# Kernel optimization log

Measured on AMD Instinct MI355X. Metric: run time of the kernel, lower is better.

## Reference

```python
import jax, jax.numpy as jnp
import numpy as np


def setup_inputs() -> dict:
    key = jax.random.key(0)
    kq, kk, kv = jax.random.split(key, 3)
    B, H, T, D = 2, 8, 8192, 64
    return {
        "Q": jax.random.normal(kq, (B, H, T, D), dtype=jnp.float32),
        "K": jax.random.normal(kk, (B, H, T, D), dtype=jnp.float32),
        "V": jax.random.normal(kv, (B, H, T, D), dtype=jnp.float32),
        "window_size": 512,
    }


def _gather_bands(x, nb, Wn):
    # x: [B,H,T,D] -> [B,H,nb,3*Wn,D], key blocks (i-1, i, i+1) per query block i
    B, H, T, D = x.shape
    xb = x.reshape(B, H, nb, Wn, D)
    xp = jnp.pad(xb, ((0, 0), (0, 0), (1, 1), (0, 0), (0, 0)))
    return jnp.concatenate([xp[:, :, i:i + nb] for i in range(3)], axis=3)


def reference(Q, K, V, window_size):
    # Sliding-window attention: softmax over keys with |q_idx - kv_idx| <= window_size,
    # computed block-sparsely (only the 3 neighboring key blocks per query block).
    B, H, T, D = Q.shape
    Wn = int(window_size)
    assert T % Wn == 0
    nb = T // Wn
    scale = 1.0 / (D ** 0.5)

    Qb = Q.reshape(B, H, nb, Wn, D)
    Kw = _gather_bands(K, nb, Wn)  # [B,H,nb,3W,D]
    Vw = _gather_bands(V, nb, Wn)

    # scores within the band: [B,H,nb,W,3W]
    s = jnp.einsum('bhnqd,bhnkd->bhnqk', Qb, Kw) * scale

    # exact band mask: global q = n*W + q_loc, global kv = (n-1)*W + k_loc
    q_loc = jnp.arange(Wn)[:, None]
    k_loc = jnp.arange(3 * Wn)[None, :]
    band = jnp.abs(q_loc + Wn - k_loc) <= Wn          # [W, 3W]
    kv_g = (jnp.arange(nb)[:, None] - 1) * Wn + jnp.arange(3 * Wn)[None, :]  # [nb, 3W]
    valid = (kv_g >= 0) & (kv_g < T)
    mask = band[None, :, :] & valid[:, None, :]        # [nb, W, 3W]

    s = jnp.where(mask[None, None], s, -jnp.inf)
    p = jax.nn.softmax(s, axis=-1)
    o = jnp.einsum('bhnqk,bhnkd->bhnqd', p, Vw)
    return o.reshape(B, H, T, D)
```

## Files before the change

kernel.cpp:

```cpp
#include <hip/hip_runtime.h>
#include <hip/hip_bf16.h>
#include <stdint.h>

typedef __attribute__((ext_vector_type(8))) short bf16x8;
typedef __attribute__((ext_vector_type(4))) float f32x4;

#define T_SEQ   8192
#define D_HEAD  64
#define NHEADS  16
#define WIN     512
#define BQ      128
#define BK      64
#define NTILES  (T_SEQ / BK)
#define LDSR    72
#define MASKVAL (-1.0e6f)

#define WS_NEEDED ((size_t)2 * NHEADS * T_SEQ * D_HEAD * 2)

__device__ __forceinline__ short f2bf(float f) {
    union { float f; uint32_t u; } v; v.f = f;
    return (short)((v.u + 0x7FFFu + ((v.u >> 16) & 1u)) >> 16);
}

__global__ __launch_bounds__(256, 2)
void prep_kv(const float* __restrict__ Kg, const float* __restrict__ Vg,
             short* __restrict__ Kb, short* __restrict__ Vt)
{
    __shared__ float vt[64 * 65];
    const int tid  = threadIdx.x;
    const int tile = blockIdx.x & (NTILES - 1);
    const int head = blockIdx.x >> 7;
    const size_t off = ((size_t)head * T_SEQ + (size_t)tile * BK) * D_HEAD;

    const float* ks = Kg + off;
    short* kd = Kb + off;
    #pragma unroll
    for (int i = 0; i < 4; ++i) {
        int idx = tid + 256 * i;
        float4 v = *(const float4*)(ks + idx * 4);
        short4 h = { f2bf(v.x), f2bf(v.y), f2bf(v.z), f2bf(v.w) };
        *(short4*)(kd + idx * 4) = h;
    }

    const float* vs = Vg + off;
    #pragma unroll
    for (int i = 0; i < 4; ++i) {
        int idx = tid + 256 * i;
        int row = idx >> 4, c4 = (idx & 15) << 2;
        float4 v = *(const float4*)(vs + row * D_HEAD + c4);
        *(float4*)&vt[row * 65 + c4] = v;
    }
    __syncthreads();
    short* vd = Vt + ((size_t)head * NTILES + tile) * (BK * D_HEAD);
    {
        int d = tid >> 2, kq = (tid & 3) << 4;
        short out[16];
        #pragma unroll
        for (int j = 0; j < 16; ++j) out[j] = f2bf(vt[(kq + j) * 65 + d]);
        *(bf16x8*)(vd + d * BK + kq)     = *(bf16x8*)&out[0];
        *(bf16x8*)(vd + d * BK + kq + 8) = *(bf16x8*)&out[8];
    }
}

__global__ __launch_bounds__(256, 2)
void swa_fwd(const float* __restrict__ Qg, const short* __restrict__ Kb,
             const short* __restrict__ Vt, float* __restrict__ Og)
{
    __shared__ short Ks[BK * LDSR];
    __shared__ short Vs[D_HEAD * LDSR];
    __shared__ short Ps[4 * 32 * LDSR];

    const int tid  = threadIdx.x;
    const int wave = tid >> 6;
    const int lane = tid & 63;
    const int lcol = lane & 15;
    const int quad = lane >> 4;

    const int g    = blockIdx.x;
    const int head = (g >> 3) >> 3;
    const int qt   = ((g & 7) << 3) | ((g >> 3) & 7);
    const int q0   = qt * BQ;
    const int tq   = q0 >> 6;

    const float* Qp = Qg + (size_t)head * T_SEQ * D_HEAD;
    const short* Kp = Kb + (size_t)head * T_SEQ * D_HEAD;
    float*       Op = Og + (size_t)head * T_SEQ * D_HEAD;

    const float qscale = 0.125f * 1.44269504088896340736f;
    const int qrow_w = q0 + wave * 32;

    bf16x8 qf[2][2];
    #pragma unroll
    for (int mt = 0; mt < 2; ++mt) {
        const float* qptr = Qp + (size_t)(qrow_w + mt*16 + lcol) * D_HEAD + quad * 8;
        #pragma unroll
        for (int ks = 0; ks < 2; ++ks) {
            float4 a = *(const float4*)(qptr + ks*32);
            float4 b = *(const float4*)(qptr + ks*32 + 4);
            bf16x8 f;
            f[0]=f2bf(a.x*qscale); f[1]=f2bf(a.y*qscale); f[2]=f2bf(a.z*qscale); f[3]=f2bf(a.w*qscale);
            f[4]=f2bf(b.x*qscale); f[5]=f2bf(b.y*qscale); f[6]=f2bf(b.z*qscale); f[7]=f2bf(b.w*qscale);
            qf[mt][ks] = f;
        }
    }

    f32x4 oacc[2][4];
    float l_run[2][4];
    const f32x4 zero4 = {0.f, 0.f, 0.f, 0.f};
    #pragma unroll
    for (int mt = 0; mt < 2; ++mt) {
        #pragma unroll
        for (int r = 0; r < 4; ++r) l_run[mt][r] = 0.f;
        #pragma unroll
        for (int nt = 0; nt < 4; ++nt) oacc[mt][nt] = zero4;
    }

    int t0 = (q0 - WIN) >> 6;            if (t0 < 0) t0 = 0;
    int t1 = (q0 + BQ - 1 + WIN) >> 6;   if (t1 > NTILES - 1) t1 = NTILES - 1;

    for (int t = t0; t <= t1; ++t) {
        __syncthreads();
        {
            const short* ksrc = Kp + (size_t)t * BK * D_HEAD;
            #pragma unroll
            for (int i = 0; i < 2; ++i) {
                int idx = tid + 256 * i;
                int row = idx >> 3, c = (idx & 7) << 3;
                *(bf16x8*)&Ks[row * LDSR + c] = *(const bf16x8*)(ksrc + idx * 8);
            }
            const short* vsrc = Vt + ((size_t)head * NTILES + t) * (BK * D_HEAD);
            #pragma unroll
            for (int i = 0; i < 2; ++i) {
                int idx = tid + 256 * i;
                int row = idx >> 3, c = (idx & 7) << 3;
                *(bf16x8*)&Vs[row * LDSR + c] = *(const bf16x8*)(vsrc + idx * 8);
            }
        }
        __syncthreads();

        f32x4 sc[2][4];
        #pragma unroll
        for (int mt = 0; mt < 2; ++mt)
            #pragma unroll
            for (int kt = 0; kt < 4; ++kt) sc[mt][kt] = zero4;
        #pragma unroll
        for (int kt = 0; kt < 4; ++kt) {
            #pragma unroll
            for (int ks = 0; ks < 2; ++ks) {
                bf16x8 kf = *(const bf16x8*)&Ks[(kt*16 + lcol)*LDSR + ks*32 + quad*8];
                sc[0][kt] = __builtin_amdgcn_mfma_f32_16x16x32_bf16(qf[0][ks], kf, sc[0][kt], 0,0,0);
                sc[1][kt] = __builtin_amdgcn_mfma_f32_16x16x32_bf16(qf[1][ks], kf, sc[1][kt], 0,0,0);
            }
        }

        if (t < tq - 6 || t > tq + 7) {
            const int kb = t * BK + lcol;
            #pragma unroll
            for (int mt = 0; mt < 2; ++mt) {
                const int qrow = qrow_w + mt*16 + quad*4;
                #pragma unroll
                for (int kt = 0; kt < 4; ++kt) {
                    int kg = kb + kt*16;
                    #pragma unroll
                    for (int r = 0; r < 4; ++r) {
                        int dq = (qrow + r) - kg;
                        if (dq > WIN || dq < -WIN) sc[mt][kt][r] = MASKVAL;
                    }
                }
            }
        }

        #pragma unroll
        for (int mt = 0; mt < 2; ++mt) {
            #pragma unroll
            for (int kt = 0; kt < 4; ++kt)
                #pragma unroll
                for (int r = 0; r < 4; ++r) {
                    float p = exp2f(sc[mt][kt][r]);
                    sc[mt][kt][r] = p;
                    l_run[mt][r] += p;
                }
            short* pw = &Ps[(wave*32 + mt*16 + quad*4) * LDSR];
            #pragma unroll
            for (int kt = 0; kt < 4; ++kt)
                #pragma unroll
                for (int r = 0; r < 4; ++r)
                    pw[r*LDSR + kt*16 + lcol] = f2bf(sc[mt][kt][r]);
        }

        const short* pr = &Ps[wave*32*LDSR];
        #pragma unroll
        for (int ks = 0; ks < 2; ++ks) {
            bf16x8 pf0 = *(const bf16x8*)&pr[(lcol     )*LDSR + ks*32 + quad*8];
            bf16x8 pf1 = *(const bf16x8*)&pr[(16 + lcol)*LDSR + ks*32 + quad*8];
            #pragma unroll
            for (int nt = 0; nt < 4; ++nt) {
                bf16x8 vf = *(const bf16x8*)&Vs[(nt*16 + lcol)*LDSR + ks*32 + quad*8];
                oacc[0][nt] = __builtin_amdgcn_mfma_f32_16x16x32_bf16(pf0, vf, oacc[0][nt], 0,0,0);
                oacc[1][nt] = __builtin_amdgcn_mfma_f32_16x16x32_bf16(pf1, vf, oacc[1][nt], 0,0,0);
            }
        }
    }

    #pragma unroll
    for (int mt = 0; mt < 2; ++mt)
        #pragma unroll
        for (int r = 0; r < 4; ++r) {
            #pragma unroll
            for (int off = 1; off < 16; off <<= 1)
                l_run[mt][r] += __shfl_xor(l_run[mt][r], off, 64);
            int row = qrow_w + mt*16 + quad*4 + r;
            float inv = 1.0f / l_run[mt][r];
            float* op = Op + (size_t)row * D_HEAD + lcol;
            #pragma unroll
            for (int nt = 0; nt < 4; ++nt)
                op[nt*16] = oacc[mt][nt][r] * inv;
        }
}

#define M_INIT  (-1.0e4f)
__global__ __launch_bounds__(256, 2)
void swa_fwd_fb(const float* __restrict__ Qg, const float* __restrict__ Kg,
                const float* __restrict__ Vg, float* __restrict__ Og)
{
    __shared__ short Ks[BK * LDSR];
    __shared__ short Vs[D_HEAD * LDSR];
    __shared__ short Ps[4 * 32 * LDSR];

    const int tid  = threadIdx.x;
    const int wave = tid >> 6;
    const int lane = tid & 63;
    const int lcol = lane & 15;
    const int quad = lane >> 4;

    const int g    = blockIdx.x;
    const int head = (g >> 3) >> 3;
    const int qt   = ((g & 7) << 3) | ((g >> 3) & 7);
    const int q0   = qt * BQ;

    const size_t base = (size_t)head * T_SEQ * D_HEAD;
    const float* Qp = Qg + base;
    const float* Kp = Kg + base;
    const float* Vp = Vg + base;
    float*       Op = Og + base;

    const float qscale = 0.125f * 1.44269504088896340736f;
    const int qrow_w = q0 + wave * 32;

    bf16x8 qf[2][2];
    #pragma unroll
    for (int mt = 0; mt < 2; ++mt) {
        const float* qptr = Qp + (size_t)(qrow_w + mt*16 + lcol) * D_HEAD + quad * 8;
        #pragma unroll
        for (int ks = 0; ks < 2; ++ks) {
            float4 a = *(const float4*)(qptr + ks*32);
            float4 b = *(const float4*)(qptr + ks*32 + 4);
            bf16x8 f;
            f[0]=f2bf(a.x*qscale); f[1]=f2bf(a.y*qscale); f[2]=f2bf(a.z*qscale); f[3]=f2bf(a.w*qscale);
            f[4]=f2bf(b.x*qscale); f[5]=f2bf(b.y*qscale); f[6]=f2bf(b.z*qscale); f[7]=f2bf(b.w*qscale);
            qf[mt][ks] = f;
        }
    }

    f32x4 oacc[2][4];
    float m_run[2][4], l_run[2][4];
    const f32x4 zero4 = {0.f, 0.f, 0.f, 0.f};
    #pragma unroll
    for (int mt = 0; mt < 2; ++mt) {
        #pragma unroll
        for (int r = 0; r < 4; ++r) { m_run[mt][r] = M_INIT; l_run[mt][r] = 0.f; }
        #pragma unroll
        for (int nt = 0; nt < 4; ++nt) oacc[mt][nt] = zero4;
    }

    int t0 = (q0 - WIN) >> 6;            if (t0 < 0) t0 = 0;
    int t1 = (q0 + BQ - 1 + WIN) >> 6;   if (t1 > NTILES - 1) t1 = NTILES - 1;

    for (int t = t0; t <= t1; ++t) {
        __syncthreads();
        {
            const float* src = Kp + (size_t)t * BK * D_HEAD;
            #pragma unroll
            for (int i = 0; i < 4; ++i) {
                int f4 = tid + 256*i;
                int row = f4 >> 4, c4 = (f4 & 15) << 2;
                float4 v = *(const float4*)(src + row*D_HEAD + c4);
                short4 h = { f2bf(v.x), f2bf(v.y), f2bf(v.z), f2bf(v.w) };
                *(short4*)&Ks[row*LDSR + c4] = h;
            }
            const float* vsrc = Vp + (size_t)t * BK * D_HEAD;
            int col = tid & 63, rb = (tid >> 6) << 2;
            #pragma unroll
            for (int i = 0; i < 4; ++i) {
                int r = rb + 16*i;
                short4 h = { f2bf(vsrc[(r+0)*D_HEAD + col]),
                             f2bf(vsrc[(r+1)*D_HEAD + col]),
                             f2bf(vsrc[(r+2)*D_HEAD + col]),
                             f2bf(vsrc[(r+3)*D_HEAD + col]) };
                *(short4*)&Vs[col*LDSR + r] = h;
            }
        }
        __syncthreads();

        f32x4 sc[2][4];
        #pragma unroll
        for (int mt = 0; mt < 2; ++mt)
            #pragma unroll
            for (int kt = 0; kt < 4; ++kt) sc[mt][kt] = zero4;
        #pragma unroll
        for (int kt = 0; kt < 4; ++kt) {
            #pragma unroll
            for (int ks = 0; ks < 2; ++ks) {
                bf16x8 kf = *(const bf16x8*)&Ks[(kt*16 + lcol)*LDSR + ks*32 + quad*8];
                sc[0][kt] = __builtin_amdgcn_mfma_f32_16x16x32_bf16(qf[0][ks], kf, sc[0][kt], 0,0,0);
                sc[1][kt] = __builtin_amdgcn_mfma_f32_16x16x32_bf16(qf[1][ks], kf, sc[1][kt], 0,0,0);
            }
        }

        const int kb = t * BK + lcol;
        #pragma unroll
        for (int mt = 0; mt < 2; ++mt) {
            const int qrow = qrow_w + mt*16 + quad*4;
            #pragma unroll
            for (int kt = 0; kt < 4; ++kt) {
                int kg = kb + kt*16;
                #pragma unroll
                for (int r = 0; r < 4; ++r) {
                    int dq = (qrow + r) - kg;
                    if (dq > WIN || dq < -WIN) sc[mt][kt][r] = MASKVAL;
                }
            }
            float tm[4], al[4], rs[4];
            #pragma unroll
            for (int r = 0; r < 4; ++r)
                tm[r] = fmaxf(fmaxf(sc[mt][0][r], sc[mt][1][r]), fmaxf(sc[mt][2][r], sc[mt][3][r]));
            #pragma unroll
            for (int off = 1; off < 16; off <<= 1)
                #pragma unroll
                for (int r = 0; r < 4; ++r)
                    tm[r] = fmaxf(tm[r], __shfl_xor(tm[r], off, 64));
            #pragma unroll
            for (int r = 0; r < 4; ++r) {
                float mn = fmaxf(m_run[mt][r], tm[r]);
                al[r] = exp2f(m_run[mt][r] - mn);
                m_run[mt][r] = mn;
                rs[r] = 0.f;
            }
            #pragma unroll
            for (int kt = 0; kt < 4; ++kt)
                #pragma unroll
                for (int r = 0; r < 4; ++r) {
                    float p = exp2f(sc[mt][kt][r] - m_run[mt][r]);
                    sc[mt][kt][r] = p;
                    rs[r] += p;
                }
            #pragma unroll
            for (int off = 1; off < 16; off <<= 1)
                #pragma unroll
                for (int r = 0; r < 4; ++r)
                    rs[r] += __shfl_xor(rs[r], off, 64);
            #pragma unroll
            for (int r = 0; r < 4; ++r)
                l_run[mt][r] = l_run[mt][r]*al[r] + rs[r];
            #pragma unroll
            for (int nt = 0; nt < 4; ++nt)
                #pragma unroll
                for (int r = 0; r < 4; ++r) oacc[mt][nt][r] *= al[r];
            short* pw = &Ps[(wave*32 + mt*16 + quad*4) * LDSR];
            #pragma unroll
            for (int kt = 0; kt < 4; ++kt)
                #pragma unroll
                for (int r = 0; r < 4; ++r)
                    pw[r*LDSR + kt*16 + lcol] = f2bf(sc[mt][kt][r]);
        }

        const short* pr = &Ps[wave*32*LDSR];
        #pragma unroll
        for (int ks = 0; ks < 2; ++ks) {
            bf16x8 pf0 = *(const bf16x8*)&pr[(lcol     )*LDSR + ks*32 + quad*8];
            bf16x8 pf1 = *(const bf16x8*)&pr[(16 + lcol)*LDSR + ks*32 + quad*8];
            #pragma unroll
            for (int nt = 0; nt < 4; ++nt) {
                bf16x8 vf = *(const bf16x8*)&Vs[(nt*16 + lcol)*LDSR + ks*32 + quad*8];
                oacc[0][nt] = __builtin_amdgcn_mfma_f32_16x16x32_bf16(pf0, vf, oacc[0][nt], 0,0,0);
                oacc[1][nt] = __builtin_amdgcn_mfma_f32_16x16x32_bf16(pf1, vf, oacc[1][nt], 0,0,0);
            }
        }
    }

    #pragma unroll
    for (int mt = 0; mt < 2; ++mt)
        #pragma unroll
        for (int r = 0; r < 4; ++r) {
            int row = qrow_w + mt*16 + quad*4 + r;
            float inv = 1.0f / l_run[mt][r];
            float* op = Op + (size_t)row * D_HEAD + lcol;
            #pragma unroll
            for (int nt = 0; nt < 4; ++nt)
                op[nt*16] = oacc[mt][nt][r] * inv;
        }
}

extern "C" void kernel_launch(void* const* d_in, const int* in_sizes, int n_in,
                              void* d_out, int out_size, void* d_ws, size_t ws_size,
                              hipStream_t stream)
{
    const float* Q = (const float*)d_in[0];
    const float* K = (const float*)d_in[1];
    const float* V = (const float*)d_in[2];
    float* O = (float*)d_out;

    if (ws_size >= WS_NEEDED) {
        short* Kb = (short*)d_ws;
        short* Vt = Kb + (size_t)NHEADS * T_SEQ * D_HEAD;
        prep_kv<<<dim3(NHEADS * NTILES), dim3(256), 0, stream>>>(K, V, Kb, Vt);
        swa_fwd<<<dim3(NHEADS * (T_SEQ / BQ)), dim3(256), 0, stream>>>(Q, Kb, Vt, O);
    } else {
        swa_fwd_fb<<<dim3(NHEADS * (T_SEQ / BQ)), dim3(256), 0, stream>>>(Q, K, V, O);
    }
}
```

Baseline: 209.2 us.

## Compute transposed scores to feed P directly from registers into PV MFMA

Swaps the QK^T MFMA operands so scores come out transposed (keys in rows, queries in lanes). Each lane can then pack its exp'd probabilities straight into a bf16x4 operand for 16x16x16 MFMAs against V, which removes the P round-trip through LDS and the shared Ps buffer. It also processes the key tile in two halves to cut register pressure, raises launch bounds to 4 blocks per CU, and writes the output with float4 stores. The cost is twice as many smaller-K MFMA instructions for PV and more LDS reads of V fragments.

Result: faster. 199.5 us (-4.6%).

```diff
diff --git a/kernel.cpp b/kernel.cpp
--- a/kernel.cpp
+++ b/kernel.cpp
@@ -3,6 +3,7 @@
 #include <stdint.h>
 
 typedef __attribute__((ext_vector_type(8))) short bf16x8;
+typedef __attribute__((ext_vector_type(4))) short bf16x4;
 typedef __attribute__((ext_vector_type(4))) float f32x4;
 
 #define T_SEQ   8192
@@ -17,9 +18,17 @@
 
 #define WS_NEEDED ((size_t)2 * NHEADS * T_SEQ * D_HEAD * 2)
 
+#define MFMA16(a,b,c) __builtin_amdgcn_mfma_f32_16x16x16bf16_1k(a,b,c,0,0,0)
+
 __device__ __forceinline__ short f2bf(float f) {
     union { float f; uint32_t u; } v; v.f = f;
     return (short)((v.u + 0x7FFFu + ((v.u >> 16) & 1u)) >> 16);
+}
+
+__device__ __forceinline__ uint32_t pkbf2(float lo, float hi) {
+    union { __hip_bfloat162 h; uint32_t u; } c;
+    c.h = __float22bfloat162_rn(make_float2(lo, hi));
+    return c.u;
 }
 
 __global__ __launch_bounds__(256, 2)
@@ -62,13 +71,12 @@
     }
 }
 
-__global__ __launch_bounds__(256, 2)
+__global__ __launch_bounds__(256, 4)
 void swa_fwd(const float* __restrict__ Qg, const short* __restrict__ Kb,
              const short* __restrict__ Vt, float* __restrict__ Og)
 {
     __shared__ short Ks[BK * LDSR];
     __shared__ short Vs[D_HEAD * LDSR];
-    __shared__ short Ps[4 * 32 * LDSR];
 
     const int tid  = threadIdx.x;
     const int wave = tid >> 6;
@@ -105,12 +113,11 @@
     }
 
     f32x4 oacc[2][4];
-    float l_run[2][4];
+    float l_run[2];
     const f32x4 zero4 = {0.f, 0.f, 0.f, 0.f};
     #pragma unroll
     for (int mt = 0; mt < 2; ++mt) {
-        #pragma unroll
-        for (int r = 0; r < 4; ++r) l_run[mt][r] = 0.f;
+        l_run[mt] = 0.f;
         #pragma unroll
         for (int nt = 0; nt < 4; ++nt) oacc[mt][nt] = zero4;
     }
@@ -122,100 +129,89 @@
         __syncthreads();
         {
             const short* ksrc = Kp + (size_t)t * BK * D_HEAD;
+            const short* vsrc = Vt + ((size_t)head * NTILES + t) * (BK * D_HEAD);
             #pragma unroll
             for (int i = 0; i < 2; ++i) {
                 int idx = tid + 256 * i;
                 int row = idx >> 3, c = (idx & 7) << 3;
                 *(bf16x8*)&Ks[row * LDSR + c] = *(const bf16x8*)(ksrc + idx * 8);
-            }
-            const short* vsrc = Vt + ((size_t)head * NTILES + t) * (BK * D_HEAD);
-            #pragma unroll
-            for (int i = 0; i < 2; ++i) {
-                int idx = tid + 256 * i;
-                int row = idx >> 3, c = (idx & 7) << 3;
                 *(bf16x8*)&Vs[row * LDSR + c] = *(const bf16x8*)(vsrc + idx * 8);
             }
         }
         __syncthreads();
 
-        f32x4 sc[2][4];
-        #pragma unroll
-        for (int mt = 0; mt < 2; ++mt)
-            #pragma unroll
-            for (int kt = 0; kt < 4; ++kt) sc[mt][kt] = zero4;
-        #pragma unroll
-        for (int kt = 0; kt < 4; ++kt) {
+        const bool edge = (t < tq - 6) || (t > tq + 7);
+
+        #pragma unroll
+        for (int h = 0; h < 2; ++h) {
+            f32x4 sc[2][2];
+            #pragma unroll
+            for (int j = 0; j < 2; ++j) { sc[j][0] = zero4; sc[j][1] = zero4; }
             #pragma unroll
             for (int ks = 0; ks < 2; ++ks) {
-                bf16x8 kf = *(const bf16x8*)&Ks[(kt*16 + lcol)*LDSR + ks*32 + quad*8];
-                sc[0][kt] = __builtin_amdgcn_mfma_f32_16x16x32_bf16(qf[0][ks], kf, sc[0][kt], 0,0,0);
-                sc[1][kt] = __builtin_amdgcn_mfma_f32_16x16x32_bf16(qf[1][ks], kf, sc[1][kt], 0,0,0);
-            }
-        }
-
-        if (t < tq - 6 || t > tq + 7) {
-            const int kb = t * BK + lcol;
-            #pragma unroll
-            for (int mt = 0; mt < 2; ++mt) {
-                const int qrow = qrow_w + mt*16 + quad*4;
-                #pragma unroll
-                for (int kt = 0; kt < 4; ++kt) {
-                    int kg = kb + kt*16;
+                #pragma unroll
+                for (int j = 0; j < 2; ++j) {
+                    bf16x8 kf = *(const bf16x8*)&Ks[((2*h+j)*16 + lcol)*LDSR + ks*32 + quad*8];
+                    sc[j][0] = __builtin_amdgcn_mfma_f32_16x16x32_bf16(kf, qf[0][ks], sc[j][0], 0,0,0);
+                    sc[j][1] = __builtin_amdgcn_mfma_f32_16x16x32_bf16(kf, qf[1][ks], sc[j][1], 0,0,0);
+                }
+            }
+
+            if (edge) {
+                #pragma unroll
+                for (int j = 0; j < 2; ++j) {
+                    const int kg0 = t*BK + (2*h+j)*16 + quad*4;
                     #pragma unroll
-                    for (int r = 0; r < 4; ++r) {
-                        int dq = (qrow + r) - kg;
-                        if (dq > WIN || dq < -WIN) sc[mt][kt][r] = MASKVAL;
+                    for (int mt = 0; mt < 2; ++mt) {
+                        const int qg = qrow_w + mt*16 + lcol;
+                        #pragma unroll
+                        for (int r = 0; r < 4; ++r) {
+                            int dq = qg - (kg0 + r);
+                            if (dq > WIN || dq < -WIN) sc[j][mt][r] = MASKVAL;
+                        }
                     }
                 }
             }
-        }
-
-        #pragma unroll
-        for (int mt = 0; mt < 2; ++mt) {
-            #pragma unroll
-            for (int kt = 0; kt < 4; ++kt)
-                #pragma unroll
-                for (int r = 0; r < 4; ++r) {
-                    float p = exp2f(sc[mt][kt][r]);
-                    sc[mt][kt][r] = p;
-                    l_run[mt][r] += p;
+
+            #pragma unroll
+            for (int j = 0; j < 2; ++j) {
+                const int kt = 2*h + j;
+                bf16x4 vf[4];
+                #pragma unroll
+                for (int nt = 0; nt < 4; ++nt)
+                    vf[nt] = *(const bf16x4*)&Vs[(nt*16 + lcol)*LDSR + kt*16 + quad*4];
+                #pragma unroll
+                for (int mt = 0; mt < 2; ++mt) {
+                    float p0 = exp2f(sc[j][mt][0]);
+                    float p1 = exp2f(sc[j][mt][1]);
+                    float p2 = exp2f(sc[j][mt][2]);
+                    float p3 = exp2f(sc[j][mt][3]);
+                    l_run[mt] += (p0 + p1) + (p2 + p3);
+                    union { int2 i; bf16x4 v; } pf;
+                    pf.i = make_int2((int)pkbf2(p0, p1), (int)pkbf2(p2, p3));
+                    #pragma unroll
+                    for (int nt = 0; nt < 4; ++nt)
+                        oacc[mt][nt] = MFMA16(vf[nt], pf.v, oacc[mt][nt]);
                 }
-            short* pw = &Ps[(wave*32 + mt*16 + quad*4) * LDSR];
-            #pragma unroll
-            for (int kt = 0; kt < 4; ++kt)
-                #pragma unroll
-                for (int r = 0; r < 4; ++r)
-                    pw[r*LDSR + kt*16 + lcol] = f2bf(sc[mt][kt][r]);
-        }
-
-        const short* pr = &Ps[wave*32*LDSR];
-        #pragma unroll
-        for (int ks = 0; ks < 2; ++ks) {
-            bf16x8 pf0 = *(const bf16x8*)&pr[(lcol     )*LDSR + ks*32 + quad*8];
-            bf16x8 pf1 = *(const bf16x8*)&pr[(16 + lcol)*LDSR + ks*32 + quad*8];
-            #pragma unroll
-            for (int nt = 0; nt < 4; ++nt) {
-                bf16x8 vf = *(const bf16x8*)&Vs[(nt*16 + lcol)*LDSR + ks*32 + quad*8];
-                oacc[0][nt] = __builtin_amdgcn_mfma_f32_16x16x32_bf16(pf0, vf, oacc[0][nt], 0,0,0);
-                oacc[1][nt] = __builtin_amdgcn_mfma_f32_16x16x32_bf16(pf1, vf, oacc[1][nt], 0,0,0);
-            }
-        }
-    }
-
-    #pragma unroll
-    for (int mt = 0; mt < 2; ++mt)
-        #pragma unroll
-        for (int r = 0; r < 4; ++r) {
-            #pragma unroll
-            for (int off = 1; off < 16; off <<= 1)
-                l_run[mt][r] += __shfl_xor(l_run[mt][r], off, 64);
-            int row = qrow_w + mt*16 + quad*4 + r;
-            float inv = 1.0f / l_run[mt][r];
-            float* op = Op + (size_t)row * D_HEAD + lcol;
-            #pragma unroll
-            for (int nt = 0; nt < 4; ++nt)
-                op[nt*16] = oacc[mt][nt][r] * inv;
-        }
+            }
+        }
+    }
+
+    #pragma unroll
+    for (int mt = 0; mt < 2; ++mt) {
+        float l = l_run[mt];
+        l += __shfl_xor(l, 16, 64);
+        l += __shfl_xor(l, 32, 64);
+        float inv = 1.0f / l;
+        const int qg = qrow_w + mt*16 + lcol;
+        float* op = Op + (size_t)qg * D_HEAD + quad*4;
+        #pragma unroll
+        for (int nt = 0; nt < 4; ++nt) {
+            float4 o = { oacc[mt][nt][0]*inv, oacc[mt][nt][1]*inv,
+                         oacc[mt][nt][2]*inv, oacc[mt][nt][3]*inv };
+            *(float4*)(op + nt*16) = o;
+        }
+    }
 }
 
 #define M_INIT  (-1.0e4f)
```
